# Performance work log

Hardware: AMD Instinct MI355X
Metric: run time of the kernel (lower is better)

The kernel has to match this reference:

```python
import jax
import jax.numpy as jnp
import numpy as np
from jax import lax

B, NS, T, H, V = 4, 96, 8, 256, 32000
L = NS * T
N = NS + 1                    # num_nodes = num_statements + 1 (exit node)
NUM_LAYERS = NS // 16         # avg_statements_per_step = 16 -> 6 execution steps


def _lstm(c, h, x, Wx, Wh, b):
    """flax-style LSTM cell: gates in (i, f, g, o) order."""
    z = x @ Wx + h @ Wh + b
    gi, gf, gg, go = jnp.split(z, 4, axis=-1)
    c2 = jax.nn.sigmoid(gf) * c + jax.nn.sigmoid(gi) * jnp.tanh(gg)
    h2 = jax.nn.sigmoid(go) * jnp.tanh(c2)
    return c2, h2


def _forward(code_statements, code_length, embed, Wx_s, Wh_s, b_s, W_se, b_se,
             Wx_e, Wh_e, b_e, W_hk, b_hk, W_sd, b_sd, W_d1, b_d1, init_a, init_b):
    # ---- statement embedding: LSTM over the T tokens of each statement ----
    tok = embed[code_statements.astype(jnp.int32)]            # [B, L, H]
    tok = jnp.transpose(tok.reshape(B * NS, T, H), (1, 0, 2))  # [T, B*NS, H]
    c0 = jnp.zeros((B * NS, H), tok.dtype)

    def scan_fn(carry, x):
        c, hh = carry
        c, hh = _lstm(c, hh, x, Wx_s, Wh_s, b_s)
        return (c, hh), None

    (_, h_last), _ = lax.scan(scan_fn, (c0, c0), tok)
    stmt = h_last.reshape(B, NS, H)                           # [B, NS, H]

    # ---- skip encoder: pairwise segment-sum embedding for skipping i -> j ----
    node = jnp.concatenate([stmt, jnp.zeros((B, 1, H), stmt.dtype)], axis=1)  # [B,N,H]
    pref = jnp.concatenate(
        [jnp.zeros((B, 1, H), stmt.dtype), jnp.cumsum(node, axis=1)], axis=1)[:, :N]
    skip = (pref[:, None, :, :] - pref[:, :, None, :]) @ W_se + b_se  # [B,N,N,H]

    stmt_len = (code_length // T).astype(jnp.int32)           # exit node index per example

    # ---- execution loop with soft instruction pointer ----
    c = jnp.broadcast_to(init_a, (B, N, H))
    h = jnp.broadcast_to(init_b, (B, N, H))
    p = jnp.zeros((B, N)).at[:, 0].set(1.0)

    def step(c, h, p, skip_nnh, length, layer):
        # per-example: c,h [N,H]; p [N]; skip_nnh [N,N,H]; length scalar
        n = p.shape[0]
        ar = jnp.arange(n)
        if layer == 0:
            mask = jnp.zeros((n, n)).at[:, 1].set(1.0)
        elif layer == NUM_LAYERS - 1:
            mask = jnp.zeros((n, n)).at[:, length].set(1.0)   # force skip to exit
        else:
            mask = 1.0 - jnp.tri(n)                           # strictly forward skips
            mask = jnp.where(ar <= length, mask, 0.0)         # no skips past exit
            mask = mask.at[:, length].set(1.0)                # always allow exit

        # skip attention logits
        skip_keys = skip_nnh @ W_sd + b_sd                    # [N,N,H]
        h_key = h @ W_hk + b_hk                               # [N,H]
        act = jax.nn.relu(jnp.concatenate(
            [jnp.broadcast_to(h_key[:, None, :], (n, n, H)), skip_keys], axis=-1))
        skip_logits = jnp.squeeze(act @ W_d1, -1) + b_d1[0]   # [N,N]
        skip_logits = jnp.where(mask > 0, skip_logits, -jnp.inf)
        skip_p = jax.nn.softmax(skip_logits, axis=-1)

        # one LSTM skip-execution step for every (i, j) pair, vectorized
        z = skip_nnh @ Wx_e + (h @ Wh_e)[:, None, :] + b_e    # [N,N,4H]
        gi, gf, gg, go = jnp.split(z, 4, axis=-1)
        c_prop = jax.nn.sigmoid(gf) * c[:, None, :] + jax.nn.sigmoid(gi) * jnp.tanh(gg)
        h_prop = jax.nn.sigmoid(go) * jnp.tanh(c_prop)
        fwd_edge = (ar[None, :] > ar[:, None])[:, :, None]    # only j > i executes
        c_prop = jnp.where(fwd_edge, c_prop, c[:, None, :])
        h_prop = jnp.where(fwd_edge, h_prop, h[:, None, :])
        valid = (mask[:, :, None] > 0) & (p[:, None, None] > 0)
        c_prop = jnp.where(valid, c_prop, 0.0)
        h_prop = jnp.where(valid, h_prop, 0.0)

        # soft aggregation of proposals weighted by p(i) * skip_p(i -> j)
        w = skip_p * p[:, None]                               # [N,N]
        denom = (w.sum(axis=0) + 1e-7)[:, None]               # [N,1]
        c_new = jnp.einsum('ijh,ij->jh', c_prop, w) / denom
        h_new = jnp.einsum('ijh,ij->jh', h_prop, w) / denom
        p_new = p @ skip_p
        return c_new, h_new, p_new

    for layer in range(NUM_LAYERS):
        c, h, p = jax.vmap(step, in_axes=(0, 0, 0, 0, 0, None))(
            c, h, p, skip, stmt_len, layer)
    return h                                                  # [B, N, H]


def setup_inputs() -> dict:
    key = jax.random.key(0)
    ks = jax.random.split(key, 16)

    def dense(k, fi, fo):
        return jax.random.normal(k, (fi, fo)) * (1.0 / np.sqrt(fi))

    return {
        'code_statements': jax.random.randint(ks[0], (B, L), 0, V, dtype=jnp.int32),
        'code_length': jax.random.randint(ks[1], (B,), 64, L, dtype=jnp.int32),
        'embed': jax.random.normal(ks[2], (V, H)) * 0.02,
        'Wx_s': dense(ks[3], H, 4 * H), 'Wh_s': dense(ks[4], H, 4 * H),
        'b_s': jnp.zeros((4 * H,)),
        'W_se': dense(ks[5], H, H), 'b_se': jnp.zeros((H,)),
        'Wx_e': dense(ks[6], H, 4 * H), 'Wh_e': dense(ks[7], H, 4 * H),
        'b_e': jnp.zeros((4 * H,)),
        'W_hk': dense(ks[8], H, H), 'b_hk': jnp.zeros((H,)),
        'W_sd': dense(ks[9], H, H), 'b_sd': jnp.zeros((H,)),
        'W_d1': dense(ks[10], 2 * H, 1), 'b_d1': jnp.zeros((1,)),
        'init_a': jax.random.normal(ks[11], (H,)),
        'init_b': jax.random.normal(ks[12], (H,)),
    }


def reference(code_statements, code_length, embed, Wx_s, Wh_s, b_s, W_se, b_se,
              Wx_e, Wh_e, b_e, W_hk, b_hk, W_sd, b_sd, W_d1, b_d1, init_a, init_b):
    return _forward(code_statements, code_length, embed, Wx_s, Wh_s, b_s, W_se, b_se,
                    Wx_e, Wh_e, b_e, W_hk, b_hk, W_sd, b_sd, W_d1, b_d1, init_a, init_b)
```

## Files before the change

### kernel.cpp

```cpp
#include <hip/hip_runtime.h>
#include <cstddef>

#define B_   4
#define NS_  96
#define T_   8
#define H_   256
#define N_   97
#define NL_  6
#define R_   388

__device__ __forceinline__ float sigm(float x) {
    return __builtin_amdgcn_rcpf(1.0f + __builtin_amdgcn_exp2f(-1.44269504f * x));
}
__device__ __forceinline__ float tanh_f(float x) {
    return 1.0f - 2.0f * __builtin_amdgcn_rcpf(1.0f + __builtin_amdgcn_exp2f(2.88539008f * x));
}

__global__ __launch_bounds__(512) void prologue(
        const int* __restrict__ ids, const float* __restrict__ embed,
        const float* __restrict__ Wx_s, const float* __restrict__ b_s,
        const float* __restrict__ b_se, const float* __restrict__ Wx_e,
        const float* __restrict__ b_e, const float* __restrict__ W_sd,
        const float* __restrict__ b_sd, const float* __restrict__ Wh_e,
        const float* __restrict__ init_a, const float* __restrict__ init_b,
        float* __restrict__ xz, float* __restrict__ cz, float* __restrict__ ck,
        float* __restrict__ hw, float* __restrict__ c0, float* __restrict__ h0,
        float* __restrict__ p0) {
    int bid = blockIdx.x, t = threadIdx.x;
    if (bid < 384) {
        __shared__ float As[64][260];
        __shared__ int ridx[64];
        int r0 = (bid >> 3) * 64, n0 = (bid & 7) * 128;
        if (t < 64) ridx[t] = ids[r0 + t];
        __syncthreads();
#pragma unroll
        for (int m = 0; m < 8; m++) {
            int L = m * 512 + t;
            int r = L >> 6, c4 = (L & 63) * 4;
            *(float4*)&As[r][c4] = *(const float4*)(embed + (size_t)ridx[r] * 256 + c4);
        }
        __syncthreads();
        int rg = t >> 5, cg = t & 31;
        float acc[4][4] = {};
        const float* wp = Wx_s + n0 + 4 * cg;
#pragma unroll 2
        for (int kb = 0; kb < 64; kb++) {
            float4 w0 = *(const float4*)(wp + (size_t)(4 * kb + 0) * 1024);
            float4 w1 = *(const float4*)(wp + (size_t)(4 * kb + 1) * 1024);
            float4 w2 = *(const float4*)(wp + (size_t)(4 * kb + 2) * 1024);
            float4 w3 = *(const float4*)(wp + (size_t)(4 * kb + 3) * 1024);
#pragma unroll
            for (int i = 0; i < 4; i++) {
                float4 a = *(const float4*)&As[rg * 4 + i][4 * kb];
                acc[i][0] = fmaf(a.x, w0.x, acc[i][0]);
                acc[i][1] = fmaf(a.x, w0.y, acc[i][1]);
                acc[i][2] = fmaf(a.x, w0.z, acc[i][2]);
                acc[i][3] = fmaf(a.x, w0.w, acc[i][3]);
                acc[i][0] = fmaf(a.y, w1.x, acc[i][0]);
                acc[i][1] = fmaf(a.y, w1.y, acc[i][1]);
                acc[i][2] = fmaf(a.y, w1.z, acc[i][2]);
                acc[i][3] = fmaf(a.y, w1.w, acc[i][3]);
                acc[i][0] = fmaf(a.z, w2.x, acc[i][0]);
                acc[i][1] = fmaf(a.z, w2.y, acc[i][1]);
                acc[i][2] = fmaf(a.z, w2.z, acc[i][2]);
                acc[i][3] = fmaf(a.z, w2.w, acc[i][3]);
                acc[i][0] = fmaf(a.w, w3.x, acc[i][0]);
                acc[i][1] = fmaf(a.w, w3.y, acc[i][1]);
                acc[i][2] = fmaf(a.w, w3.z, acc[i][2]);
                acc[i][3] = fmaf(a.w, w3.w, acc[i][3]);
            }
        }
        int col = n0 + 4 * cg;
        float4 bv = *(const float4*)&b_s[col];
#pragma unroll
        for (int i = 0; i < 4; i++) {
            int r = r0 + rg * 4 + i;
            float4 o = make_float4(acc[i][0] + bv.x, acc[i][1] + bv.y,
                                   acc[i][2] + bv.z, acc[i][3] + bv.w);
            *(float4*)&xz[(size_t)r * 1024 + col] = o;
        }
    } else if (bid < 386) {
        int n = (bid - 384) * 512 + t;
        float acc = b_e[n];
        for (int k = 0; k < 256; k++) acc = fmaf(b_se[k], Wx_e[(size_t)k * 1024 + n], acc);
        cz[n] = acc;
    } else if (bid < 388) {
        int n = (bid - 386) * 512 + t;
        float acc = b_e[n];
        for (int k = 0; k < 256; k++) {
            acc = fmaf(b_se[k], Wx_e[(size_t)k * 1024 + n], acc);
            acc = fmaf(init_b[k], Wh_e[(size_t)k * 1024 + n], acc);
        }
        hw[n] = acc;
    } else if (bid == 388) {
        if (t < 256) {
            float acc = b_sd[t];
            for (int k = 0; k < 256; k++) acc = fmaf(b_se[k], W_sd[(size_t)k * 256 + t], acc);
            ck[t] = acc;
        }
    } else {
        int r0 = (bid - 389) * 8 + (t >> 8) * 4;
        int col = t & 255;
        float ia = init_a[col], ib = init_b[col];
#pragma unroll
        for (int rr = 0; rr < 4; rr++) {
            int row = r0 + rr;
            if (row < R_) {
                c0[(size_t)row * 256 + col] = ia;
                h0[(size_t)row * 256 + col] = ib;
                if (col == 0) p0[row] = ((row % N_) == 0) ? 1.0f : 0.0f;
            }
        }
    }
}

template<int MT>
__global__ __launch_bounds__(256) void gemm_t(const float* __restrict__ A,
        const float* __restrict__ W, const float* __restrict__ bias,
        const float* __restrict__ subQ, const float* __restrict__ pgate,
        float* __restrict__ C, int R, int NC) {
    __shared__ float As[MT][260];
    __shared__ int anyflag;
    int t = threadIdx.x;
    int n0 = blockIdx.x * 128;
    int r0 = blockIdx.y * MT;
    if (pgate) {
        if (t == 0) anyflag = 0;
        __syncthreads();
        if (t < MT && r0 + t < R && pgate[r0 + t] != 0.0f) anyflag = 1;
        __syncthreads();
        if (!anyflag) return;
    }
#pragma unroll
    for (int m = 0; m < MT / 4; m++) {
        int L = m * 256 + t;
        int r = L >> 6, c4 = (L & 63) * 4;
        int rr = r0 + r;
        float4 v = make_float4(0.f, 0.f, 0.f, 0.f);
        if (rr < R) v = *(const float4*)(A + (size_t)rr * 256 + c4);
        *(float4*)&As[r][c4] = v;
    }
    __syncthreads();
    constexpr int RT = MT / 8;
    int rg = t >> 5, cg = t & 31;
    float acc[RT][4] = {};
    const float* wp = W + n0 + 4 * cg;
#pragma unroll 2
    for (int kb = 0; kb < 64; kb++) {
        float4 w0 = *(const float4*)(wp + (size_t)(4 * kb + 0) * NC);
        float4 w1 = *(const float4*)(wp + (size_t)(4 * kb + 1) * NC);
        float4 w2 = *(const float4*)(wp + (size_t)(4 * kb + 2) * NC);
        float4 w3 = *(const float4*)(wp + (size_t)(4 * kb + 3) * NC);
#pragma unroll
        for (int i = 0; i < RT; i++) {
            float4 a = *(const float4*)&As[rg * RT + i][4 * kb];
            acc[i][0] = fmaf(a.x, w0.x, acc[i][0]);
            acc[i][1] = fmaf(a.x, w0.y, acc[i][1]);
            acc[i][2] = fmaf(a.x, w0.z, acc[i][2]);
            acc[i][3] = fmaf(a.x, w0.w, acc[i][3]);
            acc[i][0] = fmaf(a.y, w1.x, acc[i][0]);
            acc[i][1] = fmaf(a.y, w1.y, acc[i][1]);
            acc[i][2] = fmaf(a.y, w1.z, acc[i][2]);
            acc[i][3] = fmaf(a.y, w1.w, acc[i][3]);
            acc[i][0] = fmaf(a.z, w2.x, acc[i][0]);
            acc[i][1] = fmaf(a.z, w2.y, acc[i][1]);
            acc[i][2] = fmaf(a.z, w2.z, acc[i][2]);
            acc[i][3] = fmaf(a.z, w2.w, acc[i][3]);
            acc[i][0] = fmaf(a.w, w3.x, acc[i][0]);
            acc[i][1] = fmaf(a.w, w3.y, acc[i][1]);
            acc[i][2] = fmaf(a.w, w3.z, acc[i][2]);
            acc[i][3] = fmaf(a.w, w3.w, acc[i][3]);
        }
    }
    int col = n0 + 4 * cg;
    float4 bv = make_float4(0.f, 0.f, 0.f, 0.f);
    if (bias) bv = *(const float4*)&bias[col];
#pragma unroll
    for (int i = 0; i < RT; i++) {
        int r = r0 + rg * RT + i;
        if (r < R) {
            float4 o = make_float4(acc[i][0] + bv.x, acc[i][1] + bv.y,
                                   acc[i][2] + bv.z, acc[i][3] + bv.w);
            if (subQ) {
                float4 s4 = *(const float4*)(subQ + (size_t)r * NC + col);
                o.x -= s4.x; o.y -= s4.y; o.z -= s4.z; o.w -= s4.w;
            }
            *(float4*)&C[(size_t)r * NC + col] = o;
        }
    }
}

__global__ __launch_bounds__(256) void qr_kernel(const float* __restrict__ S,
        const float* __restrict__ Wx_e, const float* __restrict__ W_sd,
        const float* __restrict__ hw, float* __restrict__ q, float* __restrict__ ve0,
        float* __restrict__ r_, float* __restrict__ rT) {
    __shared__ float As[16][260];
    int t = threadIdx.x;
    int bx = blockIdx.x;
    int r0 = blockIdx.y * 16;
#pragma unroll
    for (int m = 0; m < 4; m++) {
        int L = m * 256 + t;
        int r = L >> 6, c4 = (L & 63) * 4;
        int rr = r0 + r;
        float4 v = make_float4(0.f, 0.f, 0.f, 0.f);
        if (rr < R_) v = *(const float4*)(S + (size_t)rr * 256 + c4);
        *(float4*)&As[r][c4] = v;
    }
    __syncthreads();
    bool isq = bx < 8;
    const float* W = isq ? Wx_e : W_sd;
    int NC = isq ? 1024 : 256;
    int n0 = (isq ? bx : bx - 8) * 128;
    int rg = t >> 5, cg = t & 31;
    float acc[2][4] = {};
    const float* wp = W + n0 + 4 * cg;
#pragma unroll 2
    for (int kb = 0; kb < 64; kb++) {
        float4 w0 = *(const float4*)(wp + (size_t)(4 * kb + 0) * NC);
        float4 w1 = *(const float4*)(wp + (size_t)(4 * kb + 1) * NC);
        float4 w2 = *(const float4*)(wp + (size_t)(4 * kb + 2) * NC);
        float4 w3 = *(const float4*)(wp + (size_t)(4 * kb + 3) * NC);
#pragma unroll
        for (int i = 0; i < 2; i++) {
            float4 a = *(const float4*)&As[rg * 2 + i][4 * kb];
            acc[i][0] = fmaf(a.x, w0.x, acc[i][0]);
            acc[i][1] = fmaf(a.x, w0.y, acc[i][1]);
            acc[i][2] = fmaf(a.x, w0.z, acc[i][2]);
            acc[i][3] = fmaf(a.x, w0.w, acc[i][3]);
            acc[i][0] = fmaf(a.y, w1.x, acc[i][0]);
            acc[i][1] = fmaf(a.y, w1.y, acc[i][1]);
            acc[i][2] = fmaf(a.y, w1.z, acc[i][2]);
            acc[i][3] = fmaf(a.y, w1.w, acc[i][3]);
            acc[i][0] = fmaf(a.z, w2.x, acc[i][0]);
            acc[i][1] = fmaf(a.z, w2.y, acc[i][1]);
            acc[i][2] = fmaf(a.z, w2.z, acc[i][2]);
            acc[i][3] = fmaf(a.z, w2.w, acc[i][3]);
            acc[i][0] = fmaf(a.w, w3.x, acc[i][0]);
            acc[i][1] = fmaf(a.w, w3.y, acc[i][1]);
            acc[i][2] = fmaf(a.w, w3.z, acc[i][2]);
            acc[i][3] = fmaf(a.w, w3.w, acc[i][3]);
        }
    }
    int col = n0 + 4 * cg;
#pragma unroll
    for (int i = 0; i < 2; i++) {
        int r = r0 + rg * 2 + i;
        if (r < R_) {
            float4 o = make_float4(acc[i][0], acc[i][1], acc[i][2], acc[i][3]);
            if (isq) {
                *(float4*)&q[(size_t)r * 1024 + col] = o;
                float4 hwv = *(const float4*)&hw[col];
                float4 v0 = make_float4(hwv.x - o.x, hwv.y - o.y, hwv.z - o.z, hwv.w - o.w);
                *(float4*)&ve0[(size_t)r * 1024 + col] = v0;
            } else {
                *(float4*)&r_[(size_t)r * 256 + col] = o;
                int b = r / N_, n = r - b * N_;
                rT[((size_t)b * 256 + col + 0) * 128 + n] = o.x;
                rT[((size_t)b * 256 + col + 1) * 128 + n] = o.y;
                rT[((size_t)b * 256 + col + 2) * 128 + n] = o.z;
                rT[((size_t)b * 256 + col + 3) * 128 + n] = o.w;
            }
        }
    }
}

__global__ __launch_bounds__(256) void lstm_first(const float* __restrict__ xz,
        const float* __restrict__ Wh, float* __restrict__ hbuf, float* __restrict__ cbuf) {
    __shared__ float Wh_s[256][64];
    __shared__ float h_s[32][260];
    __shared__ float zs[32][68];
    int t = threadIdx.x;
    int ct = blockIdx.x, st = blockIdx.y;
    int et0 = ct * 16, s0 = st * 32;
#pragma unroll
    for (int m = 0; m < 16; m++) {
        int L = m * 256 + t;
        int k = L >> 4, f = L & 15;
        int gg = f >> 2, qq = f & 3;
        *(float4*)&Wh_s[k][f * 4] = *(const float4*)&Wh[(size_t)k * 1024 + gg * 256 + et0 + qq * 4];
    }
    for (int seq = 0; seq < 32; seq++) {
        const float* z0 = xz + ((size_t)(s0 + seq) * T_) * 1024;
        float gi = z0[t], gg = z0[512 + t], go = z0[768 + t];
        float c0v = sigm(gi) * tanh_f(gg);
        h_s[seq][t] = sigm(go) * tanh_f(c0v);
    }
    float creg[2];
    {
        int sqA = t >> 4, e = et0 + (t & 15);
#pragma unroll
        for (int u = 0; u < 2; u++) {
            const float* z0 = xz + ((size_t)(s0 + sqA + u * 16) * T_) * 1024;
            creg[u] = sigm(z0[e]) * tanh_f(z0[512 + e]);
        }
    }
    __syncthreads();
    {
        int sp = (t >> 4) & 15, cq = t & 15;
        int g = cq >> 2, q4 = cq & 3;
        int gcol = g * 256 + et0 + q4 * 4;
        float4 a0 = *(const float4*)(xz + ((size_t)(s0 + sp) * T_ + 1) * 1024 + gcol);
        float4 a1 = *(const float4*)(xz + ((size_t)(s0 + sp + 16) * T_ + 1) * 1024 + gcol);
#pragma unroll 4
        for (int k = 0; k < 256; k++) {
            float4 w4 = *(const float4*)&Wh_s[k][cq * 4];
            float hA = h_s[sp][k];
            float hB = h_s[sp + 16][k];
            a0.x = fmaf(hA, w4.x, a0.x); a0.y = fmaf(hA, w4.y, a0.y);
            a0.z = fmaf(hA, w4.z, a0.z); a0.w = fmaf(hA, w4.w, a0.w);
            a1.x = fmaf(hB, w4.x, a1.x); a1.y = fmaf(hB, w4.y, a1.y);
            a1.z = fmaf(hB, w4.z, a1.z); a1.w = fmaf(hB, w4.w, a1.w);
        }
        *(float4*)&zs[sp][cq * 4] = a0;
        *(float4*)&zs[sp + 16][cq * 4] = a1;
    }
    __syncthreads();
    {
        int sqA = t >> 4, e = t & 15;
#pragma unroll
        for (int u = 0; u < 2; u++) {
            int seq = sqA + u * 16;
            float gi = zs[seq][e], gf = zs[seq][16 + e], gg = zs[seq][32 + e], go = zs[seq][48 + e];
            float cn = sigm(gf) * creg[u] + sigm(gi) * tanh_f(gg);
            size_t gidx = (size_t)(s0 + seq) * H_ + et0 + e;
            cbuf[gidx] = cn;
            hbuf[gidx] = sigm(go) * tanh_f(cn);
        }
    }
}

__global__ __launch_bounds__(256) void lstm_step(int step, const float* __restrict__ xz,
        const float* __restrict__ Wh, float* __restrict__ hbuf, float* __restrict__ cbuf) {
    __shared__ float Wh_s[256][64];
    __shared__ float h_s[32][260];
    __shared__ float zs[32][68];
    int t = threadIdx.x;
    int ct = blockIdx.x, st = blockIdx.y;
    int et0 = ct * 16, s0 = st * 32;
    int sp = t >> 4, cq = t & 15;
    int g = cq >> 2, q4 = cq & 3;
    int gcol = g * 256 + et0 + q4 * 4;
    float4 a0 = *(const float4*)(xz + ((size_t)(s0 + sp) * T_ + step) * 1024 + gcol);
    float4 a1 = *(const float4*)(xz + ((size_t)(s0 + sp + 16) * T_ + step) * 1024 + gcol);
#pragma unroll
    for (int m = 0; m < 16; m++) {
        int L = m * 256 + t;
        int k = L >> 4, f = L & 15;
        int gg = f >> 2, qq = f & 3;
        *(float4*)&Wh_s[k][f * 4] = *(const float4*)&Wh[(size_t)k * 1024 + gg * 256 + et0 + qq * 4];
    }
#pragma unroll
    for (int m = 0; m < 8; m++) {
        int L = m * 256 + t;
        int seq = L >> 6, c4 = (L & 63) * 4;
        *(float4*)&h_s[seq][c4] = *(const float4*)&hbuf[(size_t)(s0 + seq) * H_ + c4];
    }
    __syncthreads();
#pragma unroll 4
    for (int k = 0; k < 256; k++) {
        float4 w4 = *(const float4*)&Wh_s[k][cq * 4];
        float h0 = h_s[sp][k];
        float h1 = h_s[sp + 16][k];
        a0.x = fmaf(h0, w4.x, a0.x); a0.y = fmaf(h0, w4.y, a0.y);
        a0.z = fmaf(h0, w4.z, a0.z); a0.w = fmaf(h0, w4.w, a0.w);
        a1.x = fmaf(h1, w4.x, a1.x); a1.y = fmaf(h1, w4.y, a1.y);
        a1.z = fmaf(h1, w4.z, a1.z); a1.w = fmaf(h1, w4.w, a1.w);
    }
    *(float4*)&zs[sp][cq * 4] = a0;
    *(float4*)&zs[sp + 16][cq * 4] = a1;
    __syncthreads();
    int seqA = t >> 4, e = t & 15;
#pragma unroll
    for (int u = 0; u < 2; u++) {
        int seq = seqA + u * 16;
        float gi = zs[seq][e], gf = zs[seq][16 + e], gg = zs[seq][32 + e], go = zs[seq][48 + e];
        size_t gidx = (size_t)(s0 + seq) * H_ + et0 + e;
        float cnew = sigm(gf) * cbuf[gidx] + sigm(gi) * tanh_f(gg);
        cbuf[gidx] = cnew;
        hbuf[gidx] = sigm(go) * tanh_f(cnew);
    }
}

__global__ __launch_bounds__(1024) void cumsum_k(const float* __restrict__ stmt,
                                                 float* __restrict__ pref) {
    __shared__ float buf[96][256];
    int b = blockIdx.x, t = threadIdx.x;
#pragma unroll
    for (int m = 0; m < 6; m++) {
        int L = m * 1024 + t;
        int r = L >> 6, c4 = (L & 63) * 4;
        *(float4*)&buf[r][c4] = *(const float4*)(stmt + ((size_t)b * NS_ + r) * 256 + c4);
    }
    __syncthreads();
    if (t < 256) {
        float run = 0.0f;
        pref[((size_t)b * N_) * H_ + t] = 0.0f;
        for (int n = 1; n < N_; n++) {
            run += buf[n - 1][t];
            pref[((size_t)b * N_ + n) * H_ + t] = run;
        }
    }
}

__global__ void softmax_once(const float* __restrict__ r, const float* __restrict__ rT,
                             const float* __restrict__ ck, const float* __restrict__ Wd1,
                             const int* __restrict__ code_length,
                             float* __restrict__ spT_mid, float* __restrict__ spT0,
                             float* __restrict__ spT5) {
    __shared__ float ri[H_], ckl[H_], wd[H_];
    __shared__ float part[8][128];
    __shared__ float red[128];
    int t = threadIdx.x;
    int j = t & 127, half = t >> 7;
    int bi = blockIdx.x;
    int b = bi / N_, i = bi % N_;
    if (t < H_) {
        ri[t] = r[(size_t)bi * H_ + t];
        ckl[t] = ck[t];
        wd[t] = Wd1[256 + t];
    }
    __syncthreads();
    int len = code_length[b] / T_;
    bool valid = (j < N_) && ((j > i && j <= len) || (j == len));
    float acc = 0.0f;
    if (valid) {
        const float* rTb = rT + (size_t)b * H_ * 128 + j;
        int h0 = half * 32;
#pragma unroll 4
        for (int hh = 0; hh < 32; hh++) {
            int h = h0 + hh;
            float v = rTb[(size_t)h * 128] - ri[h] + ckl[h];
            acc = fmaf(fmaxf(v, 0.0f), wd[h], acc);
        }
    }
    part[half][j] = acc;
    __syncthreads();
    float logit = -3.0e38f;
    if (t < 128) {
        if (valid)
            logit = part[0][j] + part[1][j] + part[2][j] + part[3][j]
                  + part[4][j] + part[5][j] + part[6][j] + part[7][j];
        red[j] = logit;
    }
    __syncthreads();
    for (int off = 64; off; off >>= 1) {
        if (t < off) red[t] = fmaxf(red[t], red[t + off]);
        __syncthreads();
    }
    float m = red[0];
    __syncthreads();
    float e = (t < 128 && valid) ? __builtin_amdgcn_exp2f(1.44269504f * (logit - m)) : 0.0f;
    if (t < 128) red[j] = e;
    __syncthreads();
    for (int off = 64; off; off >>= 1) {
        if (t < off) red[t] += red[t + off];
        __syncthreads();
    }
    float s = red[0];
    if (t < 128 && j < N_) {
        size_t o = ((size_t)b * N_ + j) * 128 + i;
        spT_mid[o] = e / s;
        spT0[o] = (j == 1) ? 1.0f : 0.0f;
        spT5[o] = (j == len) ? 1.0f : 0.0f;
    }
}

__global__ __launch_bounds__(512) void aggregate(const float* __restrict__ q,
        const float* __restrict__ ve, const float* __restrict__ spT,
        const float* __restrict__ p, const float* __restrict__ cc,
        const float* __restrict__ hc, float* __restrict__ cn,
        float* __restrict__ hn, float* __restrict__ pn) {
    __shared__ float qj[1024];
    __shared__ float wcol[128];
    __shared__ float red[128];
    __shared__ int vlist[128];
    __shared__ int nv_s;
    __shared__ float parts[2][2][H_];
    int t = threadIdx.x;
    int bj = blockIdx.x;
    int b = bj / N_, j = bj - b * N_;
    if (t < 128) {
        float wv = (t < N_) ? spT[(size_t)bj * 128 + t] * p[b * N_ + t] : 0.f;
        wcol[t] = wv;
        red[t] = wv;
    }
    __syncthreads();
    if (t == 0) {
        int nv = 0;
        for (int i = 0; i < N_; i++)
            if (wcol[i] != 0.0f) vlist[nv++] = i;
        nv_s = nv;
    }
    __syncthreads();
    for (int off = 64; off; off >>= 1) {
        if (t < off) red[t] += red[t + off];
        __syncthreads();
    }
    float wsum = red[0];
    if (wsum == 0.0f) {
        if (t < 256) {
            cn[(size_t)bj * H_ + t] = 0.0f;
            hn[(size_t)bj * H_ + t] = 0.0f;
            if (t == 0) pn[bj] = 0.0f;
        }
        return;
    }
    qj[t] = q[(size_t)bj * 1024 + t];
    qj[512 + t] = q[(size_t)bj * 1024 + 512 + t];
    __syncthreads();
    int hh = t & 255, vs = t >> 8;
    int nv = nv_s;
    float ac = 0.f, ah = 0.f;
    for (int v = vs; v < nv; v += 2) {
        int i = vlist[v];
        float wv = wcol[i];
        size_t rowi = (size_t)b * N_ + i;
        if (j > i) {
            const float* vei = ve + rowi * 1024;
            float gi = qj[hh] + vei[hh];
            float gf = qj[256 + hh] + vei[256 + hh];
            float gg = qj[512 + hh] + vei[512 + hh];
            float go = qj[768 + hh] + vei[768 + hh];
            float c2 = cc[rowi * H_ + hh];
            float cp = sigm(gf) * c2 + sigm(gi) * tanh_f(gg);
            float hp = sigm(go) * tanh_f(cp);
            ac = fmaf(wv, cp, ac);
            ah = fmaf(wv, hp, ah);
        } else {
            ac = fmaf(wv, cc[rowi * H_ + hh], ac);
            ah = fmaf(wv, hc[rowi * H_ + hh], ah);
        }
    }
    parts[vs][0][hh] = ac;
    parts[vs][1][hh] = ah;
    __syncthreads();
    if (t < 256) {
        float inv = __builtin_amdgcn_rcpf(wsum + 1e-7f);
        cn[(size_t)bj * H_ + t] = (parts[0][0][t] + parts[1][0][t]) * inv;
        hn[(size_t)bj * H_ + t] = (parts[0][1][t] + parts[1][1][t]) * inv;
        if (t == 0) pn[bj] = wsum;
    }
}


extern "C" void kernel_launch(void* const* d_in, const int* in_sizes, int n_in,
                              void* d_out, int out_size, void* d_ws, size_t ws_size,
                              hipStream_t stream) {
    const int*   code_statements = (const int*)d_in[0];
    const int*   code_length = (const int*)d_in[1];
    const float* embed = (const float*)d_in[2];
    const float* Wx_s = (const float*)d_in[3];
    const float* Wh_s = (const float*)d_in[4];
    const float* b_s  = (const float*)d_in[5];
    const float* W_se = (const float*)d_in[6];
    const float* b_se = (const float*)d_in[7];
    const float* Wx_e = (const float*)d_in[8];
    const float* Wh_e = (const float*)d_in[9];
    const float* b_e  = (const float*)d_in[10];
    const float* W_sd = (const float*)d_in[13];
    const float* b_sd = (const float*)d_in[14];
    const float* W_d1 = (const float*)d_in[15];
    const float* init_a = (const float*)d_in[17];
    const float* init_b = (const float*)d_in[18];
    float* out = (float*)d_out;

    float* wsf = (float*)d_ws;
    size_t off = 0;
    auto alloc = [&](size_t n) { float* p = wsf + off; off += n; return p; };
    float* cz = alloc(1024);
    float* ck = alloc(256);
    float* hw = alloc(1024);
    float* xz = alloc((size_t)3072 * 1024);
    float* stmt = alloc(384 * 256);
    float* cls = alloc(384 * 256);
    float* pref = alloc(R_ * 256);
    float* s_   = alloc(R_ * 256);
    float* q  = alloc(R_ * 1024);
    float* r_ = alloc(R_ * 256);
    float* rT = alloc(4 * 256 * 128);
    float* ve = alloc(R_ * 1024);
    float* spT_mid = alloc(R_ * 128);
    float* spT0    = alloc(R_ * 128);
    float* spT5    = alloc(R_ * 128);
    float* p0 = alloc(R_);
    float* p1 = alloc(R_);
    float* c0 = alloc(R_ * 256);
    float* c1 = alloc(R_ * 256);
    float* h0 = alloc(R_ * 256);
    float* h1 = alloc(R_ * 256);

    prologue<<<dim3(438), 512, 0, stream>>>(code_statements, embed, Wx_s, b_s,
                                            b_se, Wx_e, b_e, W_sd, b_sd, Wh_e,
                                            init_a, init_b, xz, cz, ck, hw, c0, h0, p0);
    lstm_first<<<dim3(16, 12), 256, 0, stream>>>(xz, Wh_s, stmt, cls);
    for (int step = 2; step < T_; step++)
        lstm_step<<<dim3(16, 12), 256, 0, stream>>>(step, xz, Wh_s, stmt, cls);
    cumsum_k<<<dim3(4), 1024, 0, stream>>>(stmt, pref);
    gemm_t<16><<<dim3(2, 25), 256, 0, stream>>>(pref, W_se, nullptr, nullptr, nullptr,
                                                s_, R_, 256);
    qr_kernel<<<dim3(10, 25), 256, 0, stream>>>(s_, Wx_e, W_sd, hw, q, ve, r_, rT);
    softmax_once<<<dim3(R_), 1024, 0, stream>>>(r_, rT, ck, W_d1, code_length,
                                                spT_mid, spT0, spT5);

    for (int layer = 0; layer < NL_; layer++) {
        bool odd = (layer & 1);
        float* pc = odd ? p1 : p0;
        float* pn = odd ? p0 : p1;
        float* cc = odd ? c1 : c0;
        float* cn = odd ? c0 : c1;
        float* hc = odd ? h1 : h0;
        float* hn = odd ? h0 : h1;
        if (layer == NL_ - 1) hn = out;
        const float* spT = (layer == 0) ? spT0 : (layer == NL_ - 1) ? spT5 : spT_mid;
        aggregate<<<dim3(R_), 512, 0, stream>>>(q, ve, spT, pc, cc, hc, cn, hn, pn);
        if (layer < NL_ - 1)
            gemm_t<16><<<dim3(8, 25), 256, 0, stream>>>(hn, Wh_e, cz, q, pn,
                                                        ve, R_, 1024);
    }
}
```

Measured before the change: 412.5 us.

## Precompose W_se into Wx_e and W_sd weights in prologue; stream Wh from global in LSTM

The prologue now computes M1 = W_se·Wx_e and M2 = W_se·W_sd using extra blocks that run in parallel with the token-embedding GEMM. This removes the serial pref·W_se GEMM launch from the critical path, since qr_kernel now multiplies pref directly by the precomposed weights. The LSTM step kernels no longer stage a Wh slice in shared memory and instead read Wh float4s straight from global (L2), which cuts LDS traffic and the staging cost per launch. Several GEMM loops also move to unroll 4. Precomposing weights changes the floating-point summation order slightly.

```diff
diff --git a/kernel.cpp b/kernel.cpp
--- a/kernel.cpp
+++ b/kernel.cpp
@@ -19,36 +19,55 @@
 __global__ __launch_bounds__(512) void prologue(
         const int* __restrict__ ids, const float* __restrict__ embed,
         const float* __restrict__ Wx_s, const float* __restrict__ b_s,
-        const float* __restrict__ b_se, const float* __restrict__ Wx_e,
-        const float* __restrict__ b_e, const float* __restrict__ W_sd,
-        const float* __restrict__ b_sd, const float* __restrict__ Wh_e,
+        const float* __restrict__ W_se, const float* __restrict__ b_se,
+        const float* __restrict__ Wx_e, const float* __restrict__ b_e,
+        const float* __restrict__ W_sd, const float* __restrict__ b_sd,
+        const float* __restrict__ Wh_e,
         const float* __restrict__ init_a, const float* __restrict__ init_b,
-        float* __restrict__ xz, float* __restrict__ cz, float* __restrict__ ck,
-        float* __restrict__ hw, float* __restrict__ c0, float* __restrict__ h0,
-        float* __restrict__ p0) {
+        float* __restrict__ xz, float* __restrict__ M1, float* __restrict__ M2,
+        float* __restrict__ cz, float* __restrict__ ck, float* __restrict__ hw,
+        float* __restrict__ c0, float* __restrict__ h0, float* __restrict__ p0) {
+    __shared__ float As[64][260];
+    __shared__ int ridx[64];
     int bid = blockIdx.x, t = threadIdx.x;
-    if (bid < 384) {
-        __shared__ float As[64][260];
-        __shared__ int ridx[64];
-        int r0 = (bid >> 3) * 64, n0 = (bid & 7) * 128;
-        if (t < 64) ridx[t] = ids[r0 + t];
-        __syncthreads();
+    if (bid < 424) {
+        const float* Asrc; const float* W; float* C;
+        int r0, n0, NC; bool gather = false, haveBias = false;
+        if (bid < 384) {
+            gather = true; haveBias = true;
+            r0 = (bid >> 3) * 64; n0 = (bid & 7) * 128;
+            Asrc = nullptr; W = Wx_s; C = xz; NC = 1024;
+        } else if (bid < 416) {
+            int i = bid - 384;
+            r0 = (i >> 3) * 64; n0 = (i & 7) * 128;
+            Asrc = W_se; W = Wx_e; C = M1; NC = 1024;
+        } else {
+            int i = bid - 416;
+            r0 = (i >> 1) * 64; n0 = (i & 1) * 128;
+            Asrc = W_se; W = W_sd; C = M2; NC = 256;
+        }
+        if (gather) {
+            if (t < 64) ridx[t] = ids[r0 + t];
+            __syncthreads();
+        }
 #pragma unroll
         for (int m = 0; m < 8; m++) {
             int L = m * 512 + t;
             int r = L >> 6, c4 = (L & 63) * 4;
-            *(float4*)&As[r][c4] = *(const float4*)(embed + (size_t)ridx[r] * 256 + c4);
+            const float* ap = gather ? (embed + (size_t)ridx[r] * 256)
+                                     : (Asrc + (size_t)(r0 + r) * 256);
+            *(float4*)&As[r][c4] = *(const float4*)(ap + c4);
         }
         __syncthreads();
         int rg = t >> 5, cg = t & 31;
         float acc[4][4] = {};
-        const float* wp = Wx_s + n0 + 4 * cg;
-#pragma unroll 2
+        const float* wp = W + n0 + 4 * cg;
+#pragma unroll 4
         for (int kb = 0; kb < 64; kb++) {
-            float4 w0 = *(const float4*)(wp + (size_t)(4 * kb + 0) * 1024);
-            float4 w1 = *(const float4*)(wp + (size_t)(4 * kb + 1) * 1024);
-            float4 w2 = *(const float4*)(wp + (size_t)(4 * kb + 2) * 1024);
-            float4 w3 = *(const float4*)(wp + (size_t)(4 * kb + 3) * 1024);
+            float4 w0 = *(const float4*)(wp + (size_t)(4 * kb + 0) * NC);
+            float4 w1 = *(const float4*)(wp + (size_t)(4 * kb + 1) * NC);
+            float4 w2 = *(const float4*)(wp + (size_t)(4 * kb + 2) * NC);
+            float4 w3 = *(const float4*)(wp + (size_t)(4 * kb + 3) * NC);
 #pragma unroll
             for (int i = 0; i < 4; i++) {
                 float4 a = *(const float4*)&As[rg * 4 + i][4 * kb];
@@ -71,35 +90,36 @@
             }
         }
         int col = n0 + 4 * cg;
-        float4 bv = *(const float4*)&b_s[col];
+        float4 bv = make_float4(0.f, 0.f, 0.f, 0.f);
+        if (haveBias) bv = *(const float4*)&b_s[col];
 #pragma unroll
         for (int i = 0; i < 4; i++) {
             int r = r0 + rg * 4 + i;
             float4 o = make_float4(acc[i][0] + bv.x, acc[i][1] + bv.y,
                                    acc[i][2] + bv.z, acc[i][3] + bv.w);
-            *(float4*)&xz[(size_t)r * 1024 + col] = o;
-        }
-    } else if (bid < 386) {
-        int n = (bid - 384) * 512 + t;
+            *(float4*)&C[(size_t)r * NC + col] = o;
+        }
+    } else if (bid < 426) {
+        int n = (bid - 424) * 512 + t;
         float acc = b_e[n];
         for (int k = 0; k < 256; k++) acc = fmaf(b_se[k], Wx_e[(size_t)k * 1024 + n], acc);
         cz[n] = acc;
-    } else if (bid < 388) {
-        int n = (bid - 386) * 512 + t;
+    } else if (bid < 428) {
+        int n = (bid - 426) * 512 + t;
         float acc = b_e[n];
         for (int k = 0; k < 256; k++) {
             acc = fmaf(b_se[k], Wx_e[(size_t)k * 1024 + n], acc);
             acc = fmaf(init_b[k], Wh_e[(size_t)k * 1024 + n], acc);
         }
         hw[n] = acc;
-    } else if (bid == 388) {
+    } else if (bid == 428) {
         if (t < 256) {
             float acc = b_sd[t];
             for (int k = 0; k < 256; k++) acc = fmaf(b_se[k], W_sd[(size_t)k * 256 + t], acc);
             ck[t] = acc;
         }
     } else {
-        int r0 = (bid - 389) * 8 + (t >> 8) * 4;
+        int r0 = (bid - 429) * 8 + (t >> 8) * 4;
         int col = t & 255;
         float ia = init_a[col], ib = init_b[col];
 #pragma unroll
@@ -145,7 +165,7 @@
     int rg = t >> 5, cg = t & 31;
     float acc[RT][4] = {};
     const float* wp = W + n0 + 4 * cg;
-#pragma unroll 2
+#pragma unroll 4
     for (int kb = 0; kb < 64; kb++) {
         float4 w0 = *(const float4*)(wp + (size_t)(4 * kb + 0) * NC);
         float4 w1 = *(const float4*)(wp + (size_t)(4 * kb + 1) * NC);
@@ -191,7 +211,7 @@
 }
 
 __global__ __launch_bounds__(256) void qr_kernel(const float* __restrict__ S,
-        const float* __restrict__ Wx_e, const float* __restrict__ W_sd,
+        const float* __restrict__ M1, const float* __restrict__ M2,
         const float* __restrict__ hw, float* __restrict__ q, float* __restrict__ ve0,
         float* __restrict__ r_, float* __restrict__ rT) {
     __shared__ float As[16][260];
@@ -209,13 +229,13 @@
     }
     __syncthreads();
     bool isq = bx < 8;
-    const float* W = isq ? Wx_e : W_sd;
+    const float* W = isq ? M1 : M2;
     int NC = isq ? 1024 : 256;
     int n0 = (isq ? bx : bx - 8) * 128;
     int rg = t >> 5, cg = t & 31;
     float acc[2][4] = {};
     const float* wp = W + n0 + 4 * cg;
-#pragma unroll 2
+#pragma unroll 4
     for (int kb = 0; kb < 64; kb++) {
         float4 w0 = *(const float4*)(wp + (size_t)(4 * kb + 0) * NC);
         float4 w1 = *(const float4*)(wp + (size_t)(4 * kb + 1) * NC);
@@ -267,19 +287,14 @@
 
 __global__ __launch_bounds__(256) void lstm_first(const float* __restrict__ xz,
         const float* __restrict__ Wh, float* __restrict__ hbuf, float* __restrict__ cbuf) {
-    __shared__ float Wh_s[256][64];
     __shared__ float h_s[32][260];
     __shared__ float zs[32][68];
     int t = threadIdx.x;
     int ct = blockIdx.x, st = blockIdx.y;
     int et0 = ct * 16, s0 = st * 32;
-#pragma unroll
-    for (int m = 0; m < 16; m++) {
-        int L = m * 256 + t;
-        int k = L >> 4, f = L & 15;
-        int gg = f >> 2, qq = f & 3;
-        *(float4*)&Wh_s[k][f * 4] = *(const float4*)&Wh[(size_t)k * 1024 + gg * 256 + et0 + qq * 4];
-    }
+    int sp = t >> 4, cq = t & 15;
+    int g = cq >> 2, q4 = cq & 3;
+    int gcol = g * 256 + et0 + q4 * 4;
     for (int seq = 0; seq < 32; seq++) {
         const float* z0 = xz + ((size_t)(s0 + seq) * T_) * 1024;
         float gi = z0[t], gg = z0[512 + t], go = z0[768 + t];
@@ -288,39 +303,40 @@
     }
     float creg[2];
     {
-        int sqA = t >> 4, e = et0 + (t & 15);
+        int e = et0 + (t & 15);
 #pragma unroll
         for (int u = 0; u < 2; u++) {
-            const float* z0 = xz + ((size_t)(s0 + sqA + u * 16) * T_) * 1024;
+            const float* z0 = xz + ((size_t)(s0 + sp + u * 16) * T_) * 1024;
             creg[u] = sigm(z0[e]) * tanh_f(z0[512 + e]);
         }
     }
     __syncthreads();
+    float4 a0 = *(const float4*)(xz + ((size_t)(s0 + sp) * T_ + 1) * 1024 + gcol);
+    float4 a1 = *(const float4*)(xz + ((size_t)(s0 + sp + 16) * T_ + 1) * 1024 + gcol);
+    const float* wg = Wh + gcol;
+#pragma unroll 4
+    for (int k2 = 0; k2 < 128; k2++) {
+        float4 w0 = *(const float4*)(wg + (size_t)(2 * k2) * 1024);
+        float4 w1 = *(const float4*)(wg + (size_t)(2 * k2 + 1) * 1024);
+        float2 hA = *(const float2*)&h_s[sp][2 * k2];
+        float2 hB = *(const float2*)&h_s[sp + 16][2 * k2];
+        a0.x = fmaf(hA.x, w0.x, a0.x); a0.y = fmaf(hA.x, w0.y, a0.y);
+        a0.z = fmaf(hA.x, w0.z, a0.z); a0.w = fmaf(hA.x, w0.w, a0.w);
+        a0.x = fmaf(hA.y, w1.x, a0.x); a0.y = fmaf(hA.y, w1.y, a0.y);
+        a0.z = fmaf(hA.y, w1.z, a0.z); a0.w = fmaf(hA.y, w1.w, a0.w);
+        a1.x = fmaf(hB.x, w0.x, a1.x); a1.y = fmaf(hB.x, w0.y, a1.y);
+        a1.z = fmaf(hB.x, w0.z, a1.z); a1.w = fmaf(hB.x, w0.w, a1.w);
+        a1.x = fmaf(hB.y, w1.x, a1.x); a1.y = fmaf(hB.y, w1.y, a1.y);
+        a1.z = fmaf(hB.y, w1.z, a1.z); a1.w = fmaf(hB.y, w1.w, a1.w);
+    }
+    *(float4*)&zs[sp][cq * 4] = a0;
+    *(float4*)&zs[sp + 16][cq * 4] = a1;
+    __syncthreads();
     {
-        int sp = (t >> 4) & 15, cq = t & 15;
-        int g = cq >> 2, q4 = cq & 3;
-        int gcol = g * 256 + et0 + q4 * 4;
-        float4 a0 = *(const float4*)(xz + ((size_t)(s0 + sp) * T_ + 1) * 1024 + gcol);
-        float4 a1 = *(const float4*)(xz + ((size_t)(s0 + sp + 16) * T_ + 1) * 1024 + gcol);
-#pragma unroll 4
-        for (int k = 0; k < 256; k++) {
-            float4 w4 = *(const float4*)&Wh_s[k][cq * 4];
-            float hA = h_s[sp][k];
-            float hB = h_s[sp + 16][k];
-            a0.x = fmaf(hA, w4.x, a0.x); a0.y = fmaf(hA, w4.y, a0.y);
-            a0.z = fmaf(hA, w4.z, a0.z); a0.w = fmaf(hA, w4.w, a0.w);
-            a1.x = fmaf(hB, w4.x, a1.x); a1.y = fmaf(hB, w4.y, a1.y);
-            a1.z = fmaf(hB, w4.z, a1.z); a1.w = fmaf(hB, w4.w, a1.w);
-        }
-        *(float4*)&zs[sp][cq * 4] = a0;
-        *(float4*)&zs[sp + 16][cq * 4] = a1;
-    }
-    __syncthreads();
-    {
-        int sqA = t >> 4, e = t & 15;
+        int e = t & 15;
 #pragma unroll
         for (int u = 0; u < 2; u++) {
-            int seq = sqA + u * 16;
+            int seq = sp + u * 16;
             float gi = zs[seq][e], gf = zs[seq][16 + e], gg = zs[seq][32 + e], go = zs[seq][48 + e];
             float cn = sigm(gf) * creg[u] + sigm(gi) * tanh_f(gg);
             size_t gidx = (size_t)(s0 + seq) * H_ + et0 + e;
@@ -332,7 +348,6 @@
 
 __global__ __launch_bounds__(256) void lstm_step(int step, const float* __restrict__ xz,
         const float* __restrict__ Wh, float* __restrict__ hbuf, float* __restrict__ cbuf) {
-    __shared__ float Wh_s[256][64];
     __shared__ float h_s[32][260];
     __shared__ float zs[32][68];
     int t = threadIdx.x;
@@ -344,41 +359,42 @@
     float4 a0 = *(const float4*)(xz + ((size_t)(s0 + sp) * T_ + step) * 1024 + gcol);
     float4 a1 = *(const float4*)(xz + ((size_t)(s0 + sp + 16) * T_ + step) * 1024 + gcol);
 #pragma unroll
-    for (int m = 0; m < 16; m++) {
-        int L = m * 256 + t;
-        int k = L >> 4, f = L & 15;
-        int gg = f >> 2, qq = f & 3;
-        *(float4*)&Wh_s[k][f * 4] = *(const float4*)&Wh[(size_t)k * 1024 + gg * 256 + et0 + qq * 4];
-    }
-#pragma unroll
     for (int m = 0; m < 8; m++) {
         int L = m * 256 + t;
         int seq = L >> 6, c4 = (L & 63) * 4;
         *(float4*)&h_s[seq][c4] = *(const float4*)&hbuf[(size_t)(s0 + seq) * H_ + c4];
     }
     __syncthreads();
+    const float* wg = Wh + gcol;
 #pragma unroll 4
-    for (int k = 0; k < 256; k++) {
-        float4 w4 = *(const float4*)&Wh_s[k][cq * 4];
-        float h0 = h_s[sp][k];
-        float h1 = h_s[sp + 16][k];
-        a0.x = fmaf(h0, w4.x, a0.x); a0.y = fmaf(h0, w4.y, a0.y);
-        a0.z = fmaf(h0, w4.z, a0.z); a0.w = fmaf(h0, w4.w, a0.w);
-        a1.x = fmaf(h1, w4.x, a1.x); a1.y = fmaf(h1, w4.y, a1.y);
-        a1.z = fmaf(h1, w4.z, a1.z); a1.w = fmaf(h1, w4.w, a1.w);
+    for (int k2 = 0; k2 < 128; k2++) {
+        float4 w0 = *(const float4*)(wg + (size_t)(2 * k2) * 1024);
+        float4 w1 = *(const float4*)(wg + (size_t)(2 * k2 + 1) * 1024);
+        float2 hA = *(const float2*)&h_s[sp][2 * k2];
+        float2 hB = *(const float2*)&h_s[sp + 16][2 * k2];
+        a0.x = fmaf(hA.x, w0.x, a0.x); a0.y = fmaf(hA.x, w0.y, a0.y);
+        a0.z = fmaf(hA.x, w0.z, a0.z); a0.w = fmaf(hA.x, w0.w, a0.w);
+        a0.x = fmaf(hA.y, w1.x, a0.x); a0.y = fmaf(hA.y, w1.y, a0.y);
+        a0.z = fmaf(hA.y, w1.z, a0.z); a0.w = fmaf(hA.y, w1.w, a0.w);
+        a1.x = fmaf(hB.x, w0.x, a1.x); a1.y = fmaf(hB.x, w0.y, a1.y);
+        a1.z = fmaf(hB.x, w0.z, a1.z); a1.w = fmaf(hB.x, w0.w, a1.w);
+        a1.x = fmaf(hB.y, w1.x, a1.x); a1.y = fmaf(hB.y, w1.y, a1.y);
+        a1.z = fmaf(hB.y, w1.z, a1.z); a1.w = fmaf(hB.y, w1.w, a1.w);
     }
     *(float4*)&zs[sp][cq * 4] = a0;
     *(float4*)&zs[sp + 16][cq * 4] = a1;
     __syncthreads();
-    int seqA = t >> 4, e = t & 15;
-#pragma unroll
-    for (int u = 0; u < 2; u++) {
-        int seq = seqA + u * 16;
-        float gi = zs[seq][e], gf = zs[seq][16 + e], gg = zs[seq][32 + e], go = zs[seq][48 + e];
-        size_t gidx = (size_t)(s0 + seq) * H_ + et0 + e;
-        float cnew = sigm(gf) * cbuf[gidx] + sigm(gi) * tanh_f(gg);
-        cbuf[gidx] = cnew;
-        hbuf[gidx] = sigm(go) * tanh_f(cnew);
+    {
+        int e = t & 15;
+#pragma unroll
+        for (int u = 0; u < 2; u++) {
+            int seq = sp + u * 16;
+            float gi = zs[seq][e], gf = zs[seq][16 + e], gg = zs[seq][32 + e], go = zs[seq][48 + e];
+            size_t gidx = (size_t)(s0 + seq) * H_ + et0 + e;
+            float cnew = sigm(gf) * cbuf[gidx] + sigm(gi) * tanh_f(gg);
+            cbuf[gidx] = cnew;
+            hbuf[gidx] = sigm(go) * tanh_f(cnew);
+        }
     }
 }
 
@@ -571,11 +587,12 @@
     float* cz = alloc(1024);
     float* ck = alloc(256);
     float* hw = alloc(1024);
+    float* M1 = alloc(256 * 1024);
+    float* M2 = alloc(256 * 256);
     float* xz = alloc((size_t)3072 * 1024);
     float* stmt = alloc(384 * 256);
     float* cls = alloc(384 * 256);
     float* pref = alloc(R_ * 256);
-    float* s_   = alloc(R_ * 256);
     float* q  = alloc(R_ * 1024);
     float* r_ = alloc(R_ * 256);
     float* rT = alloc(4 * 256 * 128);
@@ -590,16 +607,15 @@
     float* h0 = alloc(R_ * 256);
     float* h1 = alloc(R_ * 256);
 
-    prologue<<<dim3(438), 512, 0, stream>>>(code_statements, embed, Wx_s, b_s,
-                                            b_se, Wx_e, b_e, W_sd, b_sd, Wh_e,
-                                            init_a, init_b, xz, cz, ck, hw, c0, h0, p0);
+    prologue<<<dim3(478), 512, 0, stream>>>(code_statements, embed, Wx_s, b_s,
+                                            W_se, b_se, Wx_e, b_e, W_sd, b_sd, Wh_e,
+                                            init_a, init_b, xz, M1, M2, cz, ck, hw,
+                                            c0, h0, p0);
     lstm_first<<<dim3(16, 12), 256, 0, stream>>>(xz, Wh_s, stmt, cls);
     for (int step = 2; step < T_; step++)
         lstm_step<<<dim3(16, 12), 256, 0, stream>>>(step, xz, Wh_s, stmt, cls);
     cumsum_k<<<dim3(4), 1024, 0, stream>>>(stmt, pref);
-    gemm_t<16><<<dim3(2, 25), 256, 0, stream>>>(pref, W_se, nullptr, nullptr, nullptr,
-                                                s_, R_, 256);
-    qr_kernel<<<dim3(10, 25), 256, 0, stream>>>(s_, Wx_e, W_sd, hw, q, ve, r_, rT);
+    qr_kernel<<<dim3(10, 25), 256, 0, stream>>>(pref, M1, M2, hw, q, ve, r_, rT);
     softmax_once<<<dim3(R_), 1024, 0, stream>>>(r_, rT, ck, W_d1, code_length,
                                                 spT_mid, spT0, spT5);
 
```

Result: no change. 417.9 us (+1.3%).
